# Kernel optimization log

Measured on AMD Instinct MI355X. Metric: run time of the kernel, lower is better.

Reference implementation:

```python
import jax, jax.numpy as jnp
import numpy as np

NEG = -1e9

def setup_inputs() -> dict:
    key = jax.random.key(0)
    ks = jax.random.split(key, 6)
    B, T, H = 32, 2048, 1024
    dec = jax.random.normal(ks[0], (B, H), dtype=jnp.float32)
    enc = jax.random.normal(ks[1], (B, T, H), dtype=jnp.float32)
    mask = jax.random.randint(ks[2], (B, T), 0, 2).astype(jnp.int32)
    scale = 1.0 / np.sqrt(H)
    W_enc = jax.random.normal(ks[3], (H, H), dtype=jnp.float32) * scale
    W_dec = jax.random.normal(ks[4], (H, H), dtype=jnp.float32) * scale
    v = jax.random.normal(ks[5], (H,), dtype=jnp.float32) * scale
    return {"decoder_hidden": dec, "encoder_outputs": enc, "mask": mask,
            "W_enc": W_enc, "W_dec": W_dec, "v": v}

def reference(decoder_hidden, encoder_outputs, mask, W_enc, W_dec, v):
    # enc proj: [B,T,H] @ W_enc^T ; dec proj: [B,H] @ W_dec^T broadcast over T
    enc_p = jnp.einsum('bth,oh->bto', encoder_outputs, W_enc)
    dec_p = jnp.einsum('bh,oh->bo', decoder_hidden, W_dec)[:, None, :]  # [B,1,H]
    energy = jnp.tanh(enc_p + dec_p)                                    # [B,T,H]
    scores = jnp.einsum('bth,h->bt', energy, v)                         # [B,T]
    scores = jnp.where(mask == 0, NEG, scores)
    attn_weights = jax.nn.softmax(scores, axis=1)                       # [B,T]
    context = jnp.einsum('bt,bth->bh', attn_weights, encoder_outputs)   # [B,H]
    return (context, attn_weights)
```

## Files before the change

### kernel.cpp

```cpp
#include <hip/hip_runtime.h>
#include <hip/hip_bf16.h>
#include <stdint.h>

#define B_ 32
#define T_ 2048
#define H_ 1024
#define M_ (B_*T_)

typedef __bf16 bf16x8 __attribute__((ext_vector_type(8)));
typedef float  f32x4  __attribute__((ext_vector_type(4)));
typedef float  f32x16 __attribute__((ext_vector_type(16)));

__device__ __forceinline__ float tanh_fast(float x) {
    float e = __expf(2.0f * x);
    return 1.0f - 2.0f / (e + 1.0f);
}

__device__ __forceinline__ bf16x8 cvt2(f32x4 f0, f32x4 f1) {
    bf16x8 h;
    h[0] = (__bf16)f0[0]; h[1] = (__bf16)f0[1]; h[2] = (__bf16)f0[2]; h[3] = (__bf16)f0[3];
    h[4] = (__bf16)f1[0]; h[5] = (__bf16)f1[1]; h[6] = (__bf16)f1[2]; h[7] = (__bf16)f1[3];
    return h;
}

__device__ __forceinline__ void gl_lds16f(const float* g, float* l) {
    __builtin_amdgcn_global_load_lds(
        (const __attribute__((address_space(1))) void*)g,
        (__attribute__((address_space(3))) void*)l, 16, 0, 0);
}

__global__ __launch_bounds__(256) void k_prep(const float* __restrict__ We,
                                              __bf16* __restrict__ Wt,
                                              const float* __restrict__ dec,
                                              const float* __restrict__ Wd,
                                              float* __restrict__ decp) {
    int bx = blockIdx.x;
    int tid = threadIdx.x;
    if (bx < 512) {
        int tg = bx * 256 + tid;
        int lane = tg & 63;
        int c = (tg >> 6) & 31;
        int s = tg >> 11;
        int o = c * 32 + (lane & 31);
        int k = s * 16 + (lane >> 5) * 8;
        const f32x4* src = (const f32x4*)&We[(size_t)o * H_ + k];
        *(bf16x8*)&Wt[(size_t)tg * 8] = cvt2(src[0], src[1]);
    } else {
        int bxd = bx - 512;
        int b = bxd & 31, oc = bxd >> 5;
        int o = oc * 64 + (tid >> 2);
        int kq = tid & 3;
        const f32x4* wr = (const f32x4*)&Wd[(size_t)o * H_ + kq * 256];
        const f32x4* dr = (const f32x4*)&dec[(size_t)b * H_ + kq * 256];
        f32x4 s4 = {0.f, 0.f, 0.f, 0.f};
#pragma unroll 8
        for (int i = 0; i < 64; ++i) s4 += wr[i] * dr[i];
        float s = s4[0] + s4[1] + s4[2] + s4[3];
        s += __shfl_xor(s, 1);
        s += __shfl_xor(s, 2);
        if (kq == 0) decp[b * H_ + o] = s;
    }
}

__global__ __launch_bounds__(256, 3) void k_scores(const float* __restrict__ enc,
                                                   const float* __restrict__ decp,
                                                   const __bf16* __restrict__ Wt,
                                                   const float* __restrict__ v,
                                                   float* __restrict__ scores_p) {
    __shared__ float A_lds[3 * 4096];
    __shared__ float red[4][64];

    const int tid = threadIdx.x;
    const int w = tid >> 6, lane = tid & 63;
    const int l5 = lane & 31, q2 = lane >> 5;

    const int bx = blockIdx.x;
    const int xs = bx & 7;
    const int q = bx >> 3;
    const int nt = q & 3;
    const int rg = (q >> 2) * 8 + xs;
    const int m0 = rg * 64;
    const int b = m0 >> 11;
    const int cg0 = nt * 8 + w * 2;

    float dp[2], vvv[2];
#pragma unroll
    for (int ct = 0; ct < 2; ++ct) {
        int col = (cg0 + ct) * 32 + l5;
        dp[ct]  = decp[b * H_ + col];
        vvv[ct] = v[col];
    }

    f32x16 acc[2][2];
#pragma unroll
    for (int rt = 0; rt < 2; ++rt)
#pragma unroll
        for (int ct = 0; ct < 2; ++ct)
#pragma unroll
            for (int g = 0; g < 16; ++g)
                acc[rt][ct][g] = dp[ct];

    const int srow = w * 16 + (lane >> 4);
    const int sof  = ((lane & 15) * 4) ^ ((srow & 7) << 2);
    const int ld0  = w * 4 * 256 + lane * 4;

#define STAGE(ck_, cb_) do { \
    _Pragma("unroll") \
    for (int i_ = 0; i_ < 4; ++i_) { \
        int row_ = srow + 4 * i_; \
        int of_  = sof ^ ((i_ & 1) << 4); \
        gl_lds16f(enc + (size_t)(m0 + row_) * H_ + (ck_) * 64 + of_, \
                  &A_lds[(cb_) * 4096 + ld0 + i_ * 256]); \
    } } while (0)

    bf16x8 bb[4][2];
#define BLOAD(ck_) do { \
    _Pragma("unroll") \
    for (int sl_ = 0; sl_ < 4; ++sl_) \
        _Pragma("unroll") \
        for (int ct_ = 0; ct_ < 2; ++ct_) \
            bb[sl_][ct_] = *(const bf16x8*)&Wt[(((size_t)((ck_) * 4 + sl_) * 32 + cg0 + ct_) * 64 + lane) * 8]; \
    } while (0)

    STAGE(0, 0);
    STAGE(1, 1);
    STAGE(2, 2);
    BLOAD(0);
    __builtin_amdgcn_sched_barrier(0);
    asm volatile("s_waitcnt vmcnt(8)" ::: "memory");
    __builtin_amdgcn_s_barrier();
    __builtin_amdgcn_sched_barrier(0);

    int cb = 0;
#pragma unroll 1
    for (int ck = 0; ck < 16; ++ck) {
        const float* bufp = &A_lds[cb * 4096];

#pragma unroll
        for (int sl = 0; sl < 4; ++sl) {
            bf16x8 a[2];
#pragma unroll
            for (int rt = 0; rt < 2; ++rt) {
                int row = rt * 32 + l5;
                int kf  = sl * 16 + q2 * 8;
                int sw  = (row & 7) << 2;
                f32x4 lo = *(const f32x4*)&bufp[row * 64 + (kf ^ sw)];
                f32x4 hi = *(const f32x4*)&bufp[row * 64 + ((kf + 4) ^ sw)];
                a[rt] = cvt2(lo, hi);
            }
            acc[0][0] = __builtin_amdgcn_mfma_f32_32x32x16_bf16(a[0], bb[sl][0], acc[0][0], 0, 0, 0);
            acc[0][1] = __builtin_amdgcn_mfma_f32_32x32x16_bf16(a[0], bb[sl][1], acc[0][1], 0, 0, 0);
            acc[1][0] = __builtin_amdgcn_mfma_f32_32x32x16_bf16(a[1], bb[sl][0], acc[1][0], 0, 0, 0);
            acc[1][1] = __builtin_amdgcn_mfma_f32_32x32x16_bf16(a[1], bb[sl][1], acc[1][1], 0, 0, 0);
        }

        __builtin_amdgcn_sched_barrier(0);
        asm volatile("" ::: "memory");
        __builtin_amdgcn_s_barrier();
        asm volatile("" ::: "memory");
        __builtin_amdgcn_sched_barrier(0);

        if (ck < 15) BLOAD(ck + 1);
        __builtin_amdgcn_sched_barrier(0);
        if (ck < 13) STAGE(ck + 3, cb);
        __builtin_amdgcn_sched_barrier(0);

        cb = cb + 1; if (cb == 3) cb = 0;
    }
#undef STAGE
#undef BLOAD

    float sp[2][16];
#pragma unroll
    for (int rt = 0; rt < 2; ++rt)
#pragma unroll
        for (int g = 0; g < 16; ++g)
            sp[rt][g] = tanh_fast(acc[rt][0][g]) * vvv[0] + tanh_fast(acc[rt][1][g]) * vvv[1];

#pragma unroll
    for (int rt = 0; rt < 2; ++rt)
#pragma unroll
        for (int g = 0; g < 16; ++g) {
            float s = sp[rt][g];
            s += __shfl_xor(s, 1);
            s += __shfl_xor(s, 2);
            s += __shfl_xor(s, 4);
            s += __shfl_xor(s, 8);
            s += __shfl_xor(s, 16);
            sp[rt][g] = s;
        }

    __syncthreads();
    if (l5 == 0) {
#pragma unroll
        for (int rt = 0; rt < 2; ++rt)
#pragma unroll
            for (int g = 0; g < 16; ++g) {
                int row = rt * 32 + (g & 3) + 8 * (g >> 2) + 4 * q2;
                red[w][row] = sp[rt][g];
            }
    }
    __syncthreads();
    if (tid < 64) {
        float s = red[0][tid] + red[1][tid] + red[2][tid] + red[3][tid];
        scores_p[nt * M_ + m0 + tid] = s;
    }
}

__global__ __launch_bounds__(256) void k_ctx(const float* __restrict__ scores_p,
                                             const int* __restrict__ mask,
                                             const float* __restrict__ enc,
                                             float* __restrict__ attn,
                                             float* __restrict__ ctxp) {
    int bx = blockIdx.x;
    int b = bx >> 4, seg = bx & 15;
    int tid = threadIdx.x;
    int w = tid >> 6, lane = tid & 63;
    __shared__ float sm[2][4];
    __shared__ float wa[128];

    float val[8];
    float mx = -3e38f;
#pragma unroll
    for (int ii = 0; ii < 8; ++ii) {
        int idx = b * T_ + tid + ii * 256;
        float s = scores_p[idx] + scores_p[M_ + idx] + scores_p[2 * M_ + idx] + scores_p[3 * M_ + idx];
        s = (mask[idx] == 0) ? -1e9f : s;
        val[ii] = s;
        mx = fmaxf(mx, s);
    }
#pragma unroll
    for (int m = 1; m <= 32; m <<= 1) mx = fmaxf(mx, __shfl_xor(mx, m));
    if (lane == 0) sm[0][w] = mx;
    __syncthreads();
    mx = fmaxf(fmaxf(sm[0][0], sm[0][1]), fmaxf(sm[0][2], sm[0][3]));
    float lsum = 0.f;
#pragma unroll
    for (int ii = 0; ii < 8; ++ii) {
        val[ii] = __expf(val[ii] - mx);
        lsum += val[ii];
    }
#pragma unroll
    for (int m = 1; m <= 32; m <<= 1) lsum += __shfl_xor(lsum, m);
    if (lane == 0) sm[1][w] = lsum;
    __syncthreads();
    float inv = 1.0f / (sm[1][0] + sm[1][1] + sm[1][2] + sm[1][3]);

    if (seg == 0) {
#pragma unroll
        for (int ii = 0; ii < 8; ++ii)
            attn[b * T_ + tid + ii * 256] = val[ii] * inv;
    }
    {
        int half = seg & 1, ii0 = seg >> 1;
        if ((tid >> 7) == half) wa[tid & 127] = val[ii0] * inv;
    }
    __syncthreads();

    int t0 = seg * 128;
    const float* ep = &enc[((size_t)b * T_ + t0) * H_ + tid * 4];
    f32x4 acc = {0.f, 0.f, 0.f, 0.f};
#pragma unroll 8
    for (int t = 0; t < 128; ++t) {
        float a = wa[t];
        acc += a * *(const f32x4*)(ep + (size_t)t * H_);
    }
    *(f32x4*)&ctxp[((size_t)(seg * B_ + b)) * H_ + tid * 4] = acc;
}

__global__ __launch_bounds__(256) void k_red(const float* __restrict__ ctxp,
                                             float* __restrict__ ctx) {
    int i = blockIdx.x * 256 + threadIdx.x;
    float s = 0.f;
#pragma unroll
    for (int sg = 0; sg < 16; ++sg)
        s += ctxp[(size_t)sg * (B_ * H_) + i];
    ctx[i] = s;
}

extern "C" void kernel_launch(void* const* d_in, const int* in_sizes, int n_in,
                              void* d_out, int out_size, void* d_ws, size_t ws_size,
                              hipStream_t stream) {
    (void)in_sizes; (void)n_in; (void)out_size; (void)ws_size;
    const float* dec  = (const float*)d_in[0];
    const float* enc  = (const float*)d_in[1];
    const int*   mask = (const int*)d_in[2];
    const float* We   = (const float*)d_in[3];
    const float* Wd   = (const float*)d_in[4];
    const float* v    = (const float*)d_in[5];

    float* out = (float*)d_out;
    char* ws = (char*)d_ws;
    float*  decp     = (float*)ws;
    float*  scores_p = (float*)(ws + 131072);
    __bf16* Wt       = (__bf16*)(ws + 131072 + 1048576);
    float*  ctxp     = (float*)(ws + 131072 + 1048576 + 2097152);

    k_prep  <<<1024, 256, 0, stream>>>(We, Wt, dec, Wd, decp);
    k_scores<<<4096, 256, 0, stream>>>(enc, decp, Wt, v, scores_p);
    k_ctx   <<<512, 256, 0, stream>>>(scores_p, mask, enc, out + B_ * H_, ctxp);
    k_red   <<<128, 256, 0, stream>>>(ctxp, out);
}
```

Baseline: 569.8 us.

## Stage encoder tiles as bf16 via registers with double-buffered LDS and streamed weights

The scores GEMM now loads encoder fp32 data into registers, converts it to bf16, and writes it into a double-buffered swizzled LDS tile. This replaces the triple-buffered fp32 global_load_lds staging, which converted to bf16 on every LDS read. Weight fragments are prefetched two k-slices ahead instead of a whole chunk at a time, and MFMA issue is wrapped in setprio. The decoder projection in the prep kernel now shares dec rows through LDS across 8 batches per block, cutting its grid size. The trade-off is higher register pressure and fewer prefetch stages for the encoder stream, which could expose more memory latency.

After: 563.3 us. Within noise of the previous version (-1.1%).

```diff
diff --git a/kernel.cpp b/kernel.cpp
--- a/kernel.cpp
+++ b/kernel.cpp
@@ -23,17 +23,12 @@
     return h;
 }
 
-__device__ __forceinline__ void gl_lds16f(const float* g, float* l) {
-    __builtin_amdgcn_global_load_lds(
-        (const __attribute__((address_space(1))) void*)g,
-        (__attribute__((address_space(3))) void*)l, 16, 0, 0);
-}
-
 __global__ __launch_bounds__(256) void k_prep(const float* __restrict__ We,
                                               __bf16* __restrict__ Wt,
                                               const float* __restrict__ dec,
                                               const float* __restrict__ Wd,
                                               float* __restrict__ decp) {
+    __shared__ float dec8[8][1024];
     int bx = blockIdx.x;
     int tid = threadIdx.x;
     if (bx < 512) {
@@ -46,19 +41,31 @@
         const f32x4* src = (const f32x4*)&We[(size_t)o * H_ + k];
         *(bf16x8*)&Wt[(size_t)tg * 8] = cvt2(src[0], src[1]);
     } else {
-        int bxd = bx - 512;
-        int b = bxd & 31, oc = bxd >> 5;
-        int o = oc * 64 + (tid >> 2);
-        int kq = tid & 3;
-        const f32x4* wr = (const f32x4*)&Wd[(size_t)o * H_ + kq * 256];
-        const f32x4* dr = (const f32x4*)&dec[(size_t)b * H_ + kq * 256];
-        f32x4 s4 = {0.f, 0.f, 0.f, 0.f};
+        int bx2 = bx - 512;
+        int oc = bx2 >> 2, bg = bx2 & 3;
+        int b0 = bg * 8;
+        {
+            int r = tid >> 5, c4 = (tid & 31) * 4;
+            const float* drp = &dec[(size_t)(b0 + r) * H_];
+#pragma unroll
+            for (int j = 0; j < 8; ++j)
+                *(f32x4*)&dec8[r][c4 + j * 128] = *(const f32x4*)&drp[c4 + j * 128];
+        }
+        __syncthreads();
+        int ol = tid & 63, bi = tid >> 6;
+        int o = oc * 64 + ol;
+        const f32x4* wr = (const f32x4*)&Wd[(size_t)o * H_];
+        const f32x4* d0 = (const f32x4*)&dec8[bi][0];
+        const f32x4* d1 = (const f32x4*)&dec8[bi + 4][0];
+        f32x4 a0 = {0.f,0.f,0.f,0.f}, a1 = {0.f,0.f,0.f,0.f};
 #pragma unroll 8
-        for (int i = 0; i < 64; ++i) s4 += wr[i] * dr[i];
-        float s = s4[0] + s4[1] + s4[2] + s4[3];
-        s += __shfl_xor(s, 1);
-        s += __shfl_xor(s, 2);
-        if (kq == 0) decp[b * H_ + o] = s;
+        for (int i = 0; i < 256; ++i) {
+            f32x4 wv = wr[i];
+            a0 += wv * d0[i];
+            a1 += wv * d1[i];
+        }
+        decp[(b0 + bi) * H_ + o]     = a0[0] + a0[1] + a0[2] + a0[3];
+        decp[(b0 + bi + 4) * H_ + o] = a1[0] + a1[1] + a1[2] + a1[3];
     }
 }
 
@@ -67,7 +74,7 @@
                                                    const __bf16* __restrict__ Wt,
                                                    const float* __restrict__ v,
                                                    float* __restrict__ scores_p) {
-    __shared__ float A_lds[3 * 4096];
+    __shared__ __bf16 A_lds[2][4096];
     __shared__ float red[4][64];
 
     const int tid = threadIdx.x;
@@ -100,75 +107,74 @@
             for (int g = 0; g < 16; ++g)
                 acc[rt][ct][g] = dp[ct];
 
-    const int srow = w * 16 + (lane >> 4);
-    const int sof  = ((lane & 15) * 4) ^ ((srow & 7) << 2);
-    const int ld0  = w * 4 * 256 + lane * 4;
-
-#define STAGE(ck_, cb_) do { \
-    _Pragma("unroll") \
-    for (int i_ = 0; i_ < 4; ++i_) { \
-        int row_ = srow + 4 * i_; \
-        int of_  = sof ^ ((i_ & 1) << 4); \
-        gl_lds16f(enc + (size_t)(m0 + row_) * H_ + (ck_) * 64 + of_, \
-                  &A_lds[(cb_) * 4096 + ld0 + i_ * 256]); \
-    } } while (0)
-
-    bf16x8 bb[4][2];
-#define BLOAD(ck_) do { \
-    _Pragma("unroll") \
-    for (int sl_ = 0; sl_ < 4; ++sl_) \
-        _Pragma("unroll") \
-        for (int ct_ = 0; ct_ < 2; ++ct_) \
-            bb[sl_][ct_] = *(const bf16x8*)&Wt[(((size_t)((ck_) * 4 + sl_) * 32 + cg0 + ct_) * 64 + lane) * 8]; \
-    } while (0)
-
-    STAGE(0, 0);
-    STAGE(1, 1);
-    STAGE(2, 2);
-    BLOAD(0);
-    __builtin_amdgcn_sched_barrier(0);
-    asm volatile("s_waitcnt vmcnt(8)" ::: "memory");
-    __builtin_amdgcn_s_barrier();
-    __builtin_amdgcn_sched_barrier(0);
-
-    int cb = 0;
+    const int sr  = w * 16 + (lane >> 2);
+    const int slp = lane & 3;
+    const float* gsrc = enc + (size_t)(m0 + sr) * H_ + slp * 16;
+    const int rtw = sr >> 5, r31 = sr & 31;
+    const int wb = ((slp * 2 + rtw) * 64 + (r31 ^ (slp << 2))) * 8;
+
+    {
+        f32x4 g0 = *(const f32x4*)(gsrc + 0);
+        f32x4 g1 = *(const f32x4*)(gsrc + 4);
+        f32x4 g2 = *(const f32x4*)(gsrc + 8);
+        f32x4 g3 = *(const f32x4*)(gsrc + 12);
+        *(bf16x8*)&A_lds[0][wb]       = cvt2(g0, g1);
+        *(bf16x8*)&A_lds[0][wb + 256] = cvt2(g2, g3);
+    }
+
+    bf16x8 bb[2][2];
+#pragma unroll
+    for (int p = 0; p < 2; ++p)
+#pragma unroll
+        for (int ct = 0; ct < 2; ++ct)
+            bb[p][ct] = *(const bf16x8*)&Wt[(((size_t)p * 32 + cg0 + ct) * 64 + lane) * 8];
+
+    __syncthreads();
+
+    int cur = 0;
 #pragma unroll 1
     for (int ck = 0; ck < 16; ++ck) {
-        const float* bufp = &A_lds[cb * 4096];
+        f32x4 g0, g1, g2, g3;
+        if (ck < 15) {
+            const float* gp = gsrc + (ck + 1) * 64;
+            g0 = *(const f32x4*)(gp + 0);
+            g1 = *(const f32x4*)(gp + 4);
+            g2 = *(const f32x4*)(gp + 8);
+            g3 = *(const f32x4*)(gp + 12);
+        }
+
+        const __bf16* buf = A_lds[cur];
 
 #pragma unroll
         for (int sl = 0; sl < 4; ++sl) {
-            bf16x8 a[2];
-#pragma unroll
-            for (int rt = 0; rt < 2; ++rt) {
-                int row = rt * 32 + l5;
-                int kf  = sl * 16 + q2 * 8;
-                int sw  = (row & 7) << 2;
-                f32x4 lo = *(const f32x4*)&bufp[row * 64 + (kf ^ sw)];
-                f32x4 hi = *(const f32x4*)&bufp[row * 64 + ((kf + 4) ^ sw)];
-                a[rt] = cvt2(lo, hi);
+            const int s = ck * 4 + sl;
+            bf16x8 a0 = *(const bf16x8*)&buf[(((sl * 2 + 0) * 64) + q2 * 32 + (l5 ^ (sl << 2))) * 8];
+            bf16x8 a1 = *(const bf16x8*)&buf[(((sl * 2 + 1) * 64) + q2 * 32 + (l5 ^ (sl << 2))) * 8];
+            bf16x8 w0 = bb[s & 1][0], w1 = bb[s & 1][1];
+
+            {
+                int sn = (s + 2) & 63;
+#pragma unroll
+                for (int ct = 0; ct < 2; ++ct)
+                    bb[s & 1][ct] = *(const bf16x8*)&Wt[(((size_t)sn * 32 + cg0 + ct) * 64 + lane) * 8];
             }
-            acc[0][0] = __builtin_amdgcn_mfma_f32_32x32x16_bf16(a[0], bb[sl][0], acc[0][0], 0, 0, 0);
-            acc[0][1] = __builtin_amdgcn_mfma_f32_32x32x16_bf16(a[0], bb[sl][1], acc[0][1], 0, 0, 0);
-            acc[1][0] = __builtin_amdgcn_mfma_f32_32x32x16_bf16(a[1], bb[sl][0], acc[1][0], 0, 0, 0);
-            acc[1][1] = __builtin_amdgcn_mfma_f32_32x32x16_bf16(a[1], bb[sl][1], acc[1][1], 0, 0, 0);
-        }
-
-        __builtin_amdgcn_sched_barrier(0);
-        asm volatile("" ::: "memory");
-        __builtin_amdgcn_s_barrier();
-        asm volatile("" ::: "memory");
-        __builtin_amdgcn_sched_barrier(0);
-
-        if (ck < 15) BLOAD(ck + 1);
-        __builtin_amdgcn_sched_barrier(0);
-        if (ck < 13) STAGE(ck + 3, cb);
-        __builtin_amdgcn_sched_barrier(0);
-
-        cb = cb + 1; if (cb == 3) cb = 0;
-    }
-#undef STAGE
-#undef BLOAD
+
+            __builtin_amdgcn_s_setprio(1);
+            acc[0][0] = __builtin_amdgcn_mfma_f32_32x32x16_bf16(a0, w0, acc[0][0], 0, 0, 0);
+            acc[0][1] = __builtin_amdgcn_mfma_f32_32x32x16_bf16(a0, w1, acc[0][1], 0, 0, 0);
+            acc[1][0] = __builtin_amdgcn_mfma_f32_32x32x16_bf16(a1, w0, acc[1][0], 0, 0, 0);
+            acc[1][1] = __builtin_amdgcn_mfma_f32_32x32x16_bf16(a1, w1, acc[1][1], 0, 0, 0);
+            __builtin_amdgcn_s_setprio(0);
+        }
+
+        if (ck < 15) {
+            __bf16* dst = A_lds[cur ^ 1];
+            *(bf16x8*)&dst[wb]       = cvt2(g0, g1);
+            *(bf16x8*)&dst[wb + 256] = cvt2(g2, g3);
+        }
+        __syncthreads();
+        cur ^= 1;
+    }
 
     float sp[2][16];
 #pragma unroll
@@ -296,7 +302,7 @@
     __bf16* Wt       = (__bf16*)(ws + 131072 + 1048576);
     float*  ctxp     = (float*)(ws + 131072 + 1048576 + 2097152);
 
-    k_prep  <<<1024, 256, 0, stream>>>(We, Wt, dec, Wd, decp);
+    k_prep  <<<576, 256, 0, stream>>>(We, Wt, dec, Wd, decp);
     k_scores<<<4096, 256, 0, stream>>>(enc, decp, Wt, v, scores_p);
     k_ctx   <<<512, 256, 0, stream>>>(scores_p, mask, enc, out + B_ * H_, ctxp);
     k_red   <<<128, 256, 0, stream>>>(ctxp, out);
```
